# Optimization experiments

Hardware: AMD Instinct MI355X
Metric: run time of the kernel (lower is better)

Reference implementation:

```python
import jax, jax.numpy as jnp
from jax import lax
import numpy as np

T = 8
TAU = 2.0       # LIFNode tau
VTH = 1.0       # v_threshold for IF and LIF
ALPHA = 2.0     # surrogate.ATan default alpha
BN_EPS = 1e-5

# --- ATan surrogate-gradient heaviside (spikingjelly semantics) ---
@jax.custom_vjp
def heaviside_atan(x):
    return (x >= 0.0).astype(x.dtype)

def _h_fwd(x):
    return heaviside_atan(x), x

def _h_bwd(x, g):
    sg = (ALPHA / 2.0) / (1.0 + (jnp.pi / 2.0 * ALPHA * x) ** 2)
    return (g * sg,)

heaviside_atan.defvjp(_h_fwd, _h_bwd)

# --- multi-step IF node: v += x; spike; hard reset to 0 ---
def if_node(x_seq):
    def step(v, x):
        v = v + x
        s = heaviside_atan(v - VTH)
        return (1.0 - s) * v, s
    return lax.scan(step, jnp.zeros_like(x_seq[0]), x_seq)[1]

# --- multi-step LIF node (decay_input=True, v_reset=0, hard reset) ---
def lif_node(x_seq):
    def step(v, x):
        v = v + (x - v) / TAU
        s = heaviside_atan(v - VTH)
        return (1.0 - s) * v, s
    return lax.scan(step, jnp.zeros_like(x_seq[0]), x_seq)[1]

def conv2d(x, w, b):
    y = lax.conv_general_dilated(x, w, (1, 1), 'SAME', dimension_numbers=('NCHW', 'OIHW', 'NCHW'))
    return y + b[None, :, None, None]

def bn(x, g, b, m, v):
    scale = g * lax.rsqrt(v + BN_EPS)
    return (x - m[None, :, None, None]) * scale[None, :, None, None] + b[None, :, None, None]

def maxpool2(x):
    return lax.reduce_window(x, -jnp.inf, lax.max, (1, 1, 2, 2), (1, 1, 2, 2), 'VALID')


def setup_inputs():
    key = jax.random.key(0)
    ks = jax.random.split(key, 8)
    B = 32
    f32 = jnp.float32
    d = {}
    d['x'] = jax.random.normal(ks[0], (B, 1, 48, 48), f32)
    d['conv1_w'] = jax.random.normal(ks[1], (128, 1, 3, 3), f32) * 0.2
    d['conv1_b'] = jnp.zeros((128,), f32)
    d['bn1_g'] = jnp.ones((128,), f32)
    d['bn1_b'] = jnp.zeros((128,), f32)
    d['bn1_m'] = jnp.zeros((128,), f32)
    d['bn1_v'] = jnp.ones((128,), f32)
    d['conv2_w'] = jax.random.normal(ks[2], (128, 128, 3, 3), f32) * 0.03
    d['conv2_b'] = jnp.zeros((128,), f32)
    d['bn2_g'] = jnp.ones((128,), f32)
    d['bn2_b'] = jnp.zeros((128,), f32)
    d['bn2_m'] = jnp.zeros((128,), f32)
    d['bn2_v'] = jnp.ones((128,), f32)
    d['fc1_w'] = jax.random.normal(ks[3], (1152, 128 * 12 * 12), f32) * 0.007
    d['fc1_b'] = jnp.zeros((1152,), f32)
    d['fc2_w'] = jax.random.normal(ks[4], (128, 1152), f32) * 0.03
    d['fc2_b'] = jnp.zeros((128,), f32)
    d['fc3_w'] = jax.random.normal(ks[5], (7, 128), f32) * 0.09
    d['fc3_b'] = jnp.zeros((7,), f32)
    return d


def reference(x, conv1_w, conv1_b, bn1_g, bn1_b, bn1_m, bn1_v,
              conv2_w, conv2_b, bn2_g, bn2_b, bn2_m, bn2_v,
              fc1_w, fc1_b, fc2_w, fc2_b, fc3_w, fc3_b):
    B = x.shape[0]
    # layer1 (single-step): conv + BN (eval-mode), dropout is identity at eval
    h = bn(conv2d(x, conv1_w, conv1_b), bn1_g, bn1_b, bn1_m, bn1_v)  # [B,128,48,48]
    # repeat over T timesteps
    x_step = jnp.broadcast_to(h, (T,) + h.shape)                      # [T,B,128,48,48]
    # layer2: IF -> maxpool -> conv -> BN -> IF -> maxpool
    s1 = if_node(x_step)                                              # [T,B,128,48,48]
    p1 = maxpool2(s1.reshape((T * B,) + s1.shape[2:]))                # [T*B,128,24,24]
    c2 = bn(conv2d(p1, conv2_w, conv2_b), bn2_g, bn2_b, bn2_m, bn2_v)
    s2 = if_node(c2.reshape((T, B) + c2.shape[1:]))                   # [T,B,128,24,24]
    p2 = maxpool2(s2.reshape((T * B,) + s2.shape[2:]))                # [T*B,128,12,12]
    # layer3: flatten -> fc -> LIF -> fc -> LIF -> fc -> LIF
    f = p2.reshape(T, B, -1)                                          # [T,B,18432]
    l1 = lif_node(jnp.einsum('tbi,oi->tbo', f, fc1_w) + fc1_b)        # [T,B,1152]
    l2 = lif_node(jnp.einsum('tbi,oi->tbo', l1, fc2_w) + fc2_b)       # [T,B,128]
    l3 = lif_node(jnp.einsum('tbi,oi->tbo', l2, fc3_w) + fc3_b)       # [T,B,7]
    return l3.mean(axis=0)                                            # [B,7]
```

## Files before the change

### kernel.cpp

```cpp
#include <hip/hip_runtime.h>
#include <hip/hip_bf16.h>


typedef float  f32x4  __attribute__((ext_vector_type(4)));
typedef __bf16 bf16x8 __attribute__((ext_vector_type(8)));

#define T_STEPS 8

static const size_t OFF_P1    = 0;
static const size_t OFF_PART  = 0;
static const size_t OFF_WT    = 44302336;
static const size_t OFF_P2    = 45481984;
static const size_t OFF_W2T   = 54919168;
static const size_t OFF_L1S   = 55508992;

__device__ __forceinline__ unsigned short bf16_rne(float f) {
  unsigned u = __builtin_bit_cast(unsigned, f);
  u += 0x7FFFu + ((u >> 16) & 1u);
  return (unsigned short)(u >> 16);
}
__device__ __forceinline__ float bf16_to_f(unsigned short h) {
  unsigned u = ((unsigned)h) << 16;
  return __builtin_bit_cast(float, u);
}

__device__ __forceinline__ void split_pair(float f0, float f1, unsigned& hi, unsigned& lo) {
  __hip_bfloat162 h2 = __float22bfloat162_rn(make_float2(f0, f1));
  unsigned uh; __builtin_memcpy(&uh, &h2, 4);
  float g0 = __builtin_bit_cast(float, uh << 16);
  float g1 = __builtin_bit_cast(float, uh & 0xFFFF0000u);
  __hip_bfloat162 l2 = __float22bfloat162_rn(make_float2(f0 - g0, f1 - g1));
  unsigned ul; __builtin_memcpy(&ul, &l2, 4);
  hi = uh;
  lo = ul;
}

__device__ __forceinline__ void lds_load16(const void* g, void* l) {
  auto* gp = reinterpret_cast<const __attribute__((address_space(1))) unsigned int*>(
      reinterpret_cast<uintptr_t>(g));
  auto* lp = reinterpret_cast<__attribute__((address_space(3))) unsigned int*>(
      reinterpret_cast<uintptr_t>(l));
  __builtin_amdgcn_global_load_lds(gp, lp, 16, 0, 0);
}

__global__ __launch_bounds__(256) void prep(const float* __restrict__ conv2_w,
                                            const float* __restrict__ fc2_w,
                                            short* __restrict__ wt_hi,
                                            short* __restrict__ wt_lo,
                                            float* __restrict__ w2t,
                                            uint4* __restrict__ p1pad4) {
  int i = blockIdx.x * 256 + threadIdx.x;
  if (i < 147456) {
    int tap = i >> 14;
    int oc  = (i >> 7) & 127;
    int ic  = i & 127;
    float wv = conv2_w[oc * 1152 + ic * 9 + tap];
    unsigned short h = bf16_rne(wv);
    wt_hi[i] = (short)h;
    wt_lo[i] = (short)bf16_rne(wv - bf16_to_f(h));
  } else if (i < 294912) {
    int j = i - 147456;
    int o = j & 127, k = j >> 7;
    w2t[j] = fc2_w[o * 1152 + k];
  } else if (i < 704512) {
    int k = i - 294912;
    int tb = k / 1600;
    int rem = k - tb * 1600;
    int pos = rem >> 4, c8 = rem & 15;
    int y, x;
    if (pos < 26)      { y = 0;  x = pos; }
    else if (pos < 52) { y = 25; x = pos - 26; }
    else { int jj = pos - 52; y = 1 + (jj >> 1); x = (jj & 1) * 25; }
    p1pad4[(tb * 676 + y * 26 + x) * 16 + c8] = make_uint4(0u, 0u, 0u, 0u);
  }
}

__global__ __launch_bounds__(128) void conv1_if_pool(
    const float* __restrict__ x, const float* __restrict__ w1, const float* __restrict__ b1,
    const float* __restrict__ g1, const float* __restrict__ be1, const float* __restrict__ m1,
    const float* __restrict__ vv1, short* __restrict__ p1) {
  __shared__ float patch[16];
  const int c  = threadIdx.x;
  const int sp = blockIdx.x;
  const int b  = blockIdx.y;
  const int oy = sp / 24, ox = sp % 24;
  if (c < 16) {
    int py = c >> 2, px = c & 3;
    int iy = 2 * oy - 1 + py, ix = 2 * ox - 1 + px;
    float v = 0.f;
    if (iy >= 0 && iy < 48 && ix >= 0 && ix < 48) v = x[b * 2304 + iy * 48 + ix];
    patch[c] = v;
  }
  __syncthreads();
  float w[9];
#pragma unroll
  for (int i = 0; i < 9; ++i) w[i] = w1[c * 9 + i];
  float scale = g1[c] * rsqrtf(vv1[c] + 1e-5f);
  float shift = (b1[c] - m1[c]) * scale + be1[c];
  float h[4];
#pragma unroll
  for (int p = 0; p < 4; ++p) {
    int py = p >> 1, px = p & 1;
    float s = 0.f;
#pragma unroll
    for (int dy = 0; dy < 3; ++dy)
#pragma unroll
      for (int dx = 0; dx < 3; ++dx) s += patch[(py + dy) * 4 + (px + dx)] * w[dy * 3 + dx];
    h[p] = s * scale + shift;
  }
  float va = 0.f, vb = 0.f, vc = 0.f, vd = 0.f;
  size_t base = ((size_t)b * 676 + (size_t)(1 + oy) * 26 + (1 + ox)) * 128 + c;
#pragma unroll
  for (int t = 0; t < T_STEPS; ++t) {
    va += h[0]; vb += h[1]; vc += h[2]; vd += h[3];
    bool s0 = va >= 1.f, s1 = vb >= 1.f, s2 = vc >= 1.f, s3 = vd >= 1.f;
    p1[base + (size_t)t * (32 * 676 * 128)] = (s0 | s1 | s2 | s3) ? (short)0x3F80 : (short)0;
    if (s0) va = 0.f; if (s1) vb = 0.f; if (s2) vc = 0.f; if (s3) vd = 0.f;
  }
}

__global__ __launch_bounds__(256, 2) void conv2_gemm(
    const short* __restrict__ p1pad, const short* __restrict__ wt_hi, const short* __restrict__ wt_lo,
    const float* __restrict__ conv2_b, const float* __restrict__ bn2_g, const float* __restrict__ bn2_b,
    const float* __restrict__ bn2_m, const float* __restrict__ bn2_v, short* __restrict__ p2) {
  __shared__ __align__(16) short lds[32768];
  short* ldsA  = lds;
  short* ldsBh = lds + 16384;
  short* ldsBl = lds + 24576;

  const int tid = threadIdx.x;
  const int lane = tid & 63;
  const int w = tid >> 6;
  const int wm = w & 1, wn = w >> 1;
  const int b = blockIdx.y;
  const int gy = blockIdx.x / 3;
  const int gx = blockIdx.x - gy * 3;

  const int g = (lane & 7) ^ (lane >> 3);
  int rowofsA[8], bofs[4];
#pragma unroll
  for (int j = 0; j < 8; ++j) {
    int r = w * 64 + j * 8 + (lane >> 3);
    int t = r >> 5, iy = (r >> 3) & 3, ix = r & 7;
    rowofsA[j] = (((t * 32 + b) * 676) + (4 * gy + iy) * 26 + (8 * gx + ix)) * 128 + g * 8;
  }
#pragma unroll
  for (int j = 0; j < 4; ++j) {
    int n = w * 32 + j * 8 + (lane >> 3);
    bofs[j] = n * 128 + g * 8;
  }

  f32x4 acc[8][4];
#pragma unroll
  for (int mi = 0; mi < 8; ++mi)
#pragma unroll
    for (int ni = 0; ni < 4; ++ni) acc[mi][ni] = (f32x4){0.f, 0.f, 0.f, 0.f};

#pragma unroll 1
  for (int s = 0; s < 18; ++s) {
    const int tap = s >> 1;
    const int kk = (s & 1) << 6;
    const int tapoff = ((tap / 3) * 26 + (tap % 3)) * 128;
    __syncthreads();
#pragma unroll
    for (int j = 0; j < 8; ++j) {
      lds_load16(p1pad + rowofsA[j] + tapoff + kk, ldsA + (w * 64 + j * 8) * 64 + lane * 8);
    }
    const int wtoff = tap * 16384 + kk;
#pragma unroll
    for (int j = 0; j < 4; ++j) {
      lds_load16(wt_hi + wtoff + bofs[j], ldsBh + (w * 32 + j * 8) * 64 + lane * 8);
      lds_load16(wt_lo + wtoff + bofs[j], ldsBl + (w * 32 + j * 8) * 64 + lane * 8);
    }
    __syncthreads();
#pragma unroll
    for (int ks = 0; ks < 2; ++ks) {
      const int cch = ks * 4 + (lane >> 4);
      bf16x8 a[8], bh[4], bl[4];
#pragma unroll
      for (int i = 0; i < 8; ++i) {
        int r = wm * 128 + i * 16 + (lane & 15);
        a[i] = *(const bf16x8*)(ldsA + r * 64 + ((cch ^ (r & 7)) * 8));
      }
#pragma unroll
      for (int i = 0; i < 4; ++i) {
        int n = wn * 64 + i * 16 + (lane & 15);
        bh[i] = *(const bf16x8*)(ldsBh + n * 64 + ((cch ^ (n & 7)) * 8));
        bl[i] = *(const bf16x8*)(ldsBl + n * 64 + ((cch ^ (n & 7)) * 8));
      }
#pragma unroll
      for (int mi = 0; mi < 8; ++mi)
#pragma unroll
        for (int ni = 0; ni < 4; ++ni) {
          acc[mi][ni] = __builtin_amdgcn_mfma_f32_16x16x32_bf16(a[mi], bh[ni], acc[mi][ni], 0, 0, 0);
          acc[mi][ni] = __builtin_amdgcn_mfma_f32_16x16x32_bf16(a[mi], bl[ni], acc[mi][ni], 0, 0, 0);
        }
    }
  }

  float sc[4], sh[4];
#pragma unroll
  for (int ni = 0; ni < 4; ++ni) {
    int oc = wn * 64 + ni * 16 + (lane & 15);
    sc[ni] = bn2_g[oc] * rsqrtf(bn2_v[oc] + 1e-5f);
    sh[ni] = (conv2_b[oc] - bn2_m[oc]) * sc[ni] + bn2_b[oc];
  }
  float* ybuf = (float*)lds;
  const int S = 132;
  float v[32];
#pragma unroll
  for (int q = 0; q < 32; ++q) v[q] = 0.f;
  unsigned short* p2u = (unsigned short*)p2;
  __syncthreads();
#pragma unroll
  for (int q = 0; q < 4; ++q) {
    if (wm == (q >> 1)) {
      const int mib = (q & 1) * 4;
#pragma unroll
      for (int ml = 0; ml < 4; ++ml)
#pragma unroll
        for (int ni = 0; ni < 4; ++ni)
#pragma unroll
          for (int r = 0; r < 4; ++r) {
            int lam = ml * 16 + ((lane >> 4) << 2) + r;
            int col = wn * 64 + ni * 16 + (lane & 15);
            ybuf[lam * S + col] = acc[mib + ml][ni][r] * sc[ni] + sh[ni];
          }
    }
    __syncthreads();
    if (tid < 128) {
      const int oc = tid;
#pragma unroll
      for (int tt = 0; tt < 2; ++tt) {
        int t = 2 * q + tt;
#pragma unroll
        for (int pooly = 0; pooly < 2; ++pooly) {
          unsigned short ov[4];
#pragma unroll
          for (int poolx = 0; poolx < 4; ++poolx) {
            bool any = false;
#pragma unroll
            for (int ry = 0; ry < 2; ++ry)
#pragma unroll
              for (int rx = 0; rx < 2; ++rx) {
                int iy = 2 * pooly + ry, ix = 2 * poolx + rx;
                float xx = ybuf[(tt * 32 + iy * 8 + ix) * S + oc];
                int qi = iy * 8 + ix;
                v[qi] += xx;
                bool ss = v[qi] >= 1.f;
                any |= ss;
                if (ss) v[qi] = 0.f;
              }
            ov[poolx] = any ? (unsigned short)0x3F80 : (unsigned short)0;
          }
          ushort4 o4; o4.x = ov[0]; o4.y = ov[1]; o4.z = ov[2]; o4.w = ov[3];
          *(ushort4*)(p2u + ((size_t)(t * 32 + b) * 128 + oc) * 144 + (2 * gy + pooly) * 12 + 4 * gx) = o4;
        }
      }
    }
    __syncthreads();
  }
}

__global__ __launch_bounds__(512) void fc1_gemm(const short* __restrict__ p2,
                                                const float* __restrict__ fc1_w,
                                                float* __restrict__ part) {
  __shared__ __align__(16) short lds[32768];
  short* ldsA = lds;
  short* ldsBh = lds + 16384;
  short* ldsBl = lds + 24576;

  const int tid = threadIdx.x;
  const int lane = tid & 63;
  const int w = tid >> 6;
  const int wm = w & 3, wn = w >> 2;
  const int n0 = blockIdx.x * 128;
  const int kb = blockIdx.y * 576;

  const int g = (lane & 7) ^ (lane >> 3);
  int aofs[4];
#pragma unroll
  for (int j = 0; j < 4; ++j) {
    int r = w * 32 + j * 8 + (lane >> 3);
    aofs[j] = r * 18432 + g * 8;
  }
  const int bn = tid >> 2;
  const int c0 = (tid & 3) * 2;
  const float* wrow = fc1_w + (size_t)(n0 + bn) * 18432 + c0 * 8;
  const int bpos0 = (c0 ^ (bn & 7)) * 8;
  const int bpos1 = ((c0 + 1) ^ (bn & 7)) * 8;

  f32x4 acc[4][4];
#pragma unroll
  for (int mi = 0; mi < 4; ++mi)
#pragma unroll
    for (int ni = 0; ni < 4; ++ni) acc[mi][ni] = (f32x4){0.f, 0.f, 0.f, 0.f};

#pragma unroll 1
  for (int s = 0; s < 9; ++s) {
    const int koff = kb + s * 64;
    __syncthreads();
#pragma unroll
    for (int j = 0; j < 4; ++j) {
      lds_load16(p2 + aofs[j] + koff, ldsA + (w * 32 + j * 8) * 64 + lane * 8);
    }
    {
      const float4* wp = (const float4*)(wrow + koff);
      float4 q0 = wp[0], q1 = wp[1], q2 = wp[2], q3 = wp[3];
      unsigned h0, h1, h2, h3, h4, h5, h6, h7;
      unsigned l0, l1, l2, l3, l4, l5, l6, l7;
      split_pair(q0.x, q0.y, h0, l0);
      split_pair(q0.z, q0.w, h1, l1);
      split_pair(q1.x, q1.y, h2, l2);
      split_pair(q1.z, q1.w, h3, l3);
      split_pair(q2.x, q2.y, h4, l4);
      split_pair(q2.z, q2.w, h5, l5);
      split_pair(q3.x, q3.y, h6, l6);
      split_pair(q3.z, q3.w, h7, l7);
      uint4 H0; H0.x = h0; H0.y = h1; H0.z = h2; H0.w = h3;
      uint4 H1; H1.x = h4; H1.y = h5; H1.z = h6; H1.w = h7;
      uint4 L0; L0.x = l0; L0.y = l1; L0.z = l2; L0.w = l3;
      uint4 L1; L1.x = l4; L1.y = l5; L1.z = l6; L1.w = l7;
      *(uint4*)(ldsBh + bn * 64 + bpos0) = H0;
      *(uint4*)(ldsBh + bn * 64 + bpos1) = H1;
      *(uint4*)(ldsBl + bn * 64 + bpos0) = L0;
      *(uint4*)(ldsBl + bn * 64 + bpos1) = L1;
    }
    __syncthreads();
#pragma unroll
    for (int ks = 0; ks < 2; ++ks) {
      bf16x8 a[4], bh[4], bl[4];
      const int cch = ks * 4 + (lane >> 4);
#pragma unroll
      for (int i = 0; i < 4; ++i) {
        int r = wm * 64 + i * 16 + (lane & 15);
        a[i] = *(const bf16x8*)(ldsA + r * 64 + ((cch ^ (r & 7)) * 8));
        int n = wn * 64 + i * 16 + (lane & 15);
        bh[i] = *(const bf16x8*)(ldsBh + n * 64 + ((cch ^ (n & 7)) * 8));
        bl[i] = *(const bf16x8*)(ldsBl + n * 64 + ((cch ^ (n & 7)) * 8));
      }
#pragma unroll
      for (int mi = 0; mi < 4; ++mi)
#pragma unroll
        for (int ni = 0; ni < 4; ++ni) {
          acc[mi][ni] = __builtin_amdgcn_mfma_f32_16x16x32_bf16(a[mi], bh[ni], acc[mi][ni], 0, 0, 0);
          acc[mi][ni] = __builtin_amdgcn_mfma_f32_16x16x32_bf16(a[mi], bl[ni], acc[mi][ni], 0, 0, 0);
        }
    }
  }
  const size_t pbase = (size_t)(blockIdx.y * 9 + blockIdx.x) * 32768;
#pragma unroll
  for (int ni = 0; ni < 4; ++ni) {
    int j = wn * 64 + ni * 16 + (lane & 15);
#pragma unroll
    for (int mi = 0; mi < 4; ++mi) {
#pragma unroll
      for (int r = 0; r < 4; ++r) {
        int m = wm * 64 + mi * 16 + ((lane >> 4) << 2) + r;
        part[pbase + (size_t)m * 128 + j] = acc[mi][ni][r];
      }
    }
  }
}

__global__ __launch_bounds__(128) void fc1_reduce_lif(const float* __restrict__ part,
                                                      const float* __restrict__ fc1_b,
                                                      float* __restrict__ l1s) {
  int i = blockIdx.x * 128 + threadIdx.x;
  int b = i / 1152, n = i - b * 1152;
  int nt = n >> 7, j = n & 127;
  float bias = fc1_b[n];
  float v = 0.f;
#pragma unroll
  for (int t = 0; t < T_STEPS; ++t) {
    int m = t * 32 + b;
    float s = bias;
#pragma unroll 8
    for (int ks = 0; ks < 32; ++ks) s += part[(((size_t)ks * 9 + nt) * 256 + m) * 128 + j];
    v += (s - v) * 0.5f;
    bool sp = v >= 1.f;
    l1s[(size_t)m * 1152 + n] = sp ? 1.f : 0.f;
    if (sp) v = 0.f;
  }
}

__global__ __launch_bounds__(512) void tail(const float* __restrict__ l1s,
                                            const float* __restrict__ w2t,
                                            const float* __restrict__ b2,
                                            const float* __restrict__ w3,
                                            const float* __restrict__ b3,
                                            float* __restrict__ out) {
  __shared__ float sx[8][1152];
  __shared__ float part2[4][8][128];
  __shared__ float s2[8][128];
  __shared__ float y3[7][8];
  const int b = blockIdx.x;
  const int tid = threadIdx.x;
  for (int i = tid; i < 9216; i += 512) {
    int t = i / 1152, k = i - t * 1152;
    sx[t][k] = l1s[(size_t)(t * 32 + b) * 1152 + k];
  }
  __syncthreads();
  const int o = tid & 127, h = tid >> 7;
  float p[8];
#pragma unroll
  for (int t = 0; t < 8; ++t) p[t] = 0.f;
#pragma unroll 4
  for (int kk = 0; kk < 288; ++kk) {
    int k = h * 288 + kk;
    float wv = w2t[k * 128 + o];
#pragma unroll
    for (int t = 0; t < 8; ++t) p[t] += sx[t][k] * wv;
  }
#pragma unroll
  for (int t = 0; t < 8; ++t) part2[h][t][o] = p[t];
  __syncthreads();
  if (tid < 128) {
    float v = 0.f;
#pragma unroll
    for (int t = 0; t < 8; ++t) {
      float xx = part2[0][t][o] + part2[1][t][o] + part2[2][t][o] + part2[3][t][o] + b2[o];
      v += (xx - v) * 0.5f;
      bool s = v >= 1.f;
      s2[t][o] = s ? 1.f : 0.f;
      if (s) v = 0.f;
    }
  }
  __syncthreads();
  if (tid < 56) {
    int oo = tid >> 3, t = tid & 7;
    float d = 0.f;
    for (int k = 0; k < 128; ++k) d += s2[t][k] * w3[oo * 128 + k];
    y3[oo][t] = d + b3[oo];
  }
  __syncthreads();
  if (tid < 7) {
    float v = 0.f, a = 0.f;
#pragma unroll
    for (int t = 0; t < 8; ++t) {
      float xx = y3[tid][t];
      v += (xx - v) * 0.5f;
      bool s = v >= 1.f;
      a += s ? 1.f : 0.f;
      if (s) v = 0.f;
    }
    out[b * 7 + tid] = a * 0.125f;
  }
}

extern "C" void kernel_launch(void* const* d_in, const int* in_sizes, int n_in,
                              void* d_out, int out_size, void* d_ws, size_t ws_size,
                              hipStream_t stream) {
  const float* x       = (const float*)d_in[0];
  const float* conv1_w = (const float*)d_in[1];
  const float* conv1_b = (const float*)d_in[2];
  const float* bn1_g   = (const float*)d_in[3];
  const float* bn1_b   = (const float*)d_in[4];
  const float* bn1_m   = (const float*)d_in[5];
  const float* bn1_v   = (const float*)d_in[6];
  const float* conv2_w = (const float*)d_in[7];
  const float* conv2_b = (const float*)d_in[8];
  const float* bn2_g   = (const float*)d_in[9];
  const float* bn2_b   = (const float*)d_in[10];
  const float* bn2_m   = (const float*)d_in[11];
  const float* bn2_v   = (const float*)d_in[12];
  const float* fc1_w   = (const float*)d_in[13];
  const float* fc1_b   = (const float*)d_in[14];
  const float* fc2_w   = (const float*)d_in[15];
  const float* fc2_b   = (const float*)d_in[16];
  const float* fc3_w   = (const float*)d_in[17];
  const float* fc3_b   = (const float*)d_in[18];

  char* ws = (char*)d_ws;
  short* p1pad = (short*)(ws + OFF_P1);
  float* part  = (float*)(ws + OFF_PART);
  short* wt_hi = (short*)(ws + OFF_WT);
  short* wt_lo = wt_hi + 147456;
  short* p2    = (short*)(ws + OFF_P2);
  float* w2t   = (float*)(ws + OFF_W2T);
  float* l1s   = (float*)(ws + OFF_L1S);
  float* out   = (float*)d_out;

  prep<<<2752, 256, 0, stream>>>(conv2_w, fc2_w, wt_hi, wt_lo, w2t, (uint4*)p1pad);
  conv1_if_pool<<<dim3(576, 32), 128, 0, stream>>>(x, conv1_w, conv1_b, bn1_g, bn1_b, bn1_m, bn1_v, p1pad);
  conv2_gemm<<<dim3(18, 32), 256, 0, stream>>>(p1pad, wt_hi, wt_lo, conv2_b, bn2_g, bn2_b, bn2_m, bn2_v, p2);
  fc1_gemm<<<dim3(9, 32), 512, 0, stream>>>(p2, fc1_w, part);
  fc1_reduce_lif<<<288, 128, 0, stream>>>(part, fc1_b, l1s);
  tail<<<32, 512, 0, stream>>>(l1s, w2t, fc2_b, fc3_w, fc3_b, out);
}
```

Before: 368.5 us.

## Double-buffer conv2 GEMM LDS stages with K=32 slices to overlap loads

Restructures the conv2 implicit-GEMM main loop from 18 K=64 stages into 36 K=32 stages using two LDS buffers. The next stage's global-to-LDS copy is issued after fragments are read and before the MFMAs, so copy latency can overlap compute, and one barrier per iteration replaces two. The LDS row stride and XOR swizzle change to fit 32-element rows. The trade-off is twice as many iterations and barriers relative to compute per stage, plus whether the lds_load16 copies actually run asynchronously.

```diff
diff --git a/kernel.cpp b/kernel.cpp
--- a/kernel.cpp
+++ b/kernel.cpp
@@ -124,9 +124,6 @@
     const float* __restrict__ conv2_b, const float* __restrict__ bn2_g, const float* __restrict__ bn2_b,
     const float* __restrict__ bn2_m, const float* __restrict__ bn2_v, short* __restrict__ p2) {
   __shared__ __align__(16) short lds[32768];
-  short* ldsA  = lds;
-  short* ldsBh = lds + 16384;
-  short* ldsBl = lds + 24576;
 
   const int tid = threadIdx.x;
   const int lane = tid & 63;
@@ -136,19 +133,39 @@
   const int gy = blockIdx.x / 3;
   const int gx = blockIdx.x - gy * 3;
 
-  const int g = (lane & 7) ^ (lane >> 3);
-  int rowofsA[8], bofs[4];
-#pragma unroll
-  for (int j = 0; j < 8; ++j) {
-    int r = w * 64 + j * 8 + (lane >> 3);
+  int rowofsA[4], bofs[2];
+#pragma unroll
+  for (int j = 0; j < 4; ++j) {
+    int r = w * 64 + j * 16 + (lane >> 2);
     int t = r >> 5, iy = (r >> 3) & 3, ix = r & 7;
-    rowofsA[j] = (((t * 32 + b) * 676) + (4 * gy + iy) * 26 + (8 * gx + ix)) * 128 + g * 8;
-  }
-#pragma unroll
-  for (int j = 0; j < 4; ++j) {
-    int n = w * 32 + j * 8 + (lane >> 3);
-    bofs[j] = n * 128 + g * 8;
-  }
+    int cA = (lane & 3) ^ ((r >> 1) & 3);
+    rowofsA[j] = (((t * 32 + b) * 676) + (4 * gy + iy) * 26 + (8 * gx + ix)) * 128 + cA * 8;
+  }
+#pragma unroll
+  for (int j = 0; j < 2; ++j) {
+    int n = w * 32 + j * 16 + (lane >> 2);
+    int cB = (lane & 3) ^ ((n >> 1) & 3);
+    bofs[j] = n * 128 + cB * 8;
+  }
+
+  auto stage = [&](int st, int bsel) {
+    const int tap = st >> 2;
+    const int kk  = (st & 3) << 5;
+    const int ty = tap / 3, tx = tap - ty * 3;
+    const int coff = (ty * 26 + tx) * 128 + kk;
+    const int woff = tap * 16384 + kk;
+    short* dst = lds + (bsel << 14);
+#pragma unroll
+    for (int j = 0; j < 4; ++j)
+      lds_load16(p1pad + rowofsA[j] + coff, dst + (w * 64 + j * 16) * 32 + lane * 8);
+#pragma unroll
+    for (int j = 0; j < 2; ++j) {
+      lds_load16(wt_hi + woff + bofs[j], dst + 8192 + (w * 32 + j * 16) * 32 + lane * 8);
+      lds_load16(wt_lo + woff + bofs[j], dst + 12288 + (w * 32 + j * 16) * 32 + lane * 8);
+    }
+  };
+
+  stage(0, 0);
 
   f32x4 acc[8][4];
 #pragma unroll
@@ -156,46 +173,35 @@
 #pragma unroll
     for (int ni = 0; ni < 4; ++ni) acc[mi][ni] = (f32x4){0.f, 0.f, 0.f, 0.f};
 
+  __syncthreads();
+
 #pragma unroll 1
-  for (int s = 0; s < 18; ++s) {
-    const int tap = s >> 1;
-    const int kk = (s & 1) << 6;
-    const int tapoff = ((tap / 3) * 26 + (tap % 3)) * 128;
+  for (int ss = 0; ss < 36; ++ss) {
+    const short* bufA  = lds + ((ss & 1) << 14);
+    const short* bufBh = bufA + 8192;
+    const short* bufBl = bufA + 12288;
+    const int cch = lane >> 4;
+    bf16x8 a[8], bh[4], bl[4];
+#pragma unroll
+    for (int i = 0; i < 8; ++i) {
+      int r = wm * 128 + i * 16 + (lane & 15);
+      a[i] = *(const bf16x8*)(bufA + r * 32 + ((cch ^ ((r >> 1) & 3)) * 8));
+    }
+#pragma unroll
+    for (int i = 0; i < 4; ++i) {
+      int n = wn * 64 + i * 16 + (lane & 15);
+      bh[i] = *(const bf16x8*)(bufBh + n * 32 + ((cch ^ ((n >> 1) & 3)) * 8));
+      bl[i] = *(const bf16x8*)(bufBl + n * 32 + ((cch ^ ((n >> 1) & 3)) * 8));
+    }
+    if (ss < 35) stage(ss + 1, (ss + 1) & 1);
+#pragma unroll
+    for (int mi = 0; mi < 8; ++mi)
+#pragma unroll
+      for (int ni = 0; ni < 4; ++ni) {
+        acc[mi][ni] = __builtin_amdgcn_mfma_f32_16x16x32_bf16(a[mi], bh[ni], acc[mi][ni], 0, 0, 0);
+        acc[mi][ni] = __builtin_amdgcn_mfma_f32_16x16x32_bf16(a[mi], bl[ni], acc[mi][ni], 0, 0, 0);
+      }
     __syncthreads();
-#pragma unroll
-    for (int j = 0; j < 8; ++j) {
-      lds_load16(p1pad + rowofsA[j] + tapoff + kk, ldsA + (w * 64 + j * 8) * 64 + lane * 8);
-    }
-    const int wtoff = tap * 16384 + kk;
-#pragma unroll
-    for (int j = 0; j < 4; ++j) {
-      lds_load16(wt_hi + wtoff + bofs[j], ldsBh + (w * 32 + j * 8) * 64 + lane * 8);
-      lds_load16(wt_lo + wtoff + bofs[j], ldsBl + (w * 32 + j * 8) * 64 + lane * 8);
-    }
-    __syncthreads();
-#pragma unroll
-    for (int ks = 0; ks < 2; ++ks) {
-      const int cch = ks * 4 + (lane >> 4);
-      bf16x8 a[8], bh[4], bl[4];
-#pragma unroll
-      for (int i = 0; i < 8; ++i) {
-        int r = wm * 128 + i * 16 + (lane & 15);
-        a[i] = *(const bf16x8*)(ldsA + r * 64 + ((cch ^ (r & 7)) * 8));
-      }
-#pragma unroll
-      for (int i = 0; i < 4; ++i) {
-        int n = wn * 64 + i * 16 + (lane & 15);
-        bh[i] = *(const bf16x8*)(ldsBh + n * 64 + ((cch ^ (n & 7)) * 8));
-        bl[i] = *(const bf16x8*)(ldsBl + n * 64 + ((cch ^ (n & 7)) * 8));
-      }
-#pragma unroll
-      for (int mi = 0; mi < 8; ++mi)
-#pragma unroll
-        for (int ni = 0; ni < 4; ++ni) {
-          acc[mi][ni] = __builtin_amdgcn_mfma_f32_16x16x32_bf16(a[mi], bh[ni], acc[mi][ni], 0, 0, 0);
-          acc[mi][ni] = __builtin_amdgcn_mfma_f32_16x16x32_bf16(a[mi], bl[ni], acc[mi][ni], 0, 0, 0);
-        }
-    }
   }
 
   float sc[4], sh[4];
```

After: 383.1 us. 1.04x slower.
